# Optimization experiments

Measured on AMD Instinct MI355X. Metric: run time of the kernel, lower is better.

The kernel has to match this reference:

```python
import jax, jax.numpy as jnp
import numpy as np

V, E, H, L, B, T = 32000, 256, 512, 2, 32, 64
SOS_TOKEN = 1


def setup_inputs() -> dict:
    key = jax.random.key(0)
    ks = jax.random.split(key, 16)
    s = 0.02
    inp = {
        'encoder_outputs': jax.random.normal(ks[0], (B, T, H), dtype=jnp.float32),
        'encoder_hidden': jax.random.normal(ks[1], (L, B, H), dtype=jnp.float32),
        'target_tensor': jax.random.randint(ks[2], (B, T), 0, V, dtype=jnp.int64),
        'embedding': jax.random.normal(ks[3], (V, E), dtype=jnp.float32) * s,
        'W_ih0': jax.random.normal(ks[4], (3 * H, E), dtype=jnp.float32) * s,
        'W_hh0': jax.random.normal(ks[5], (3 * H, H), dtype=jnp.float32) * s,
        'b_ih0': jax.random.normal(ks[6], (3 * H,), dtype=jnp.float32) * s,
        'b_hh0': jax.random.normal(ks[7], (3 * H,), dtype=jnp.float32) * s,
        'W_ih1': jax.random.normal(ks[8], (3 * H, H), dtype=jnp.float32) * s,
        'W_hh1': jax.random.normal(ks[9], (3 * H, H), dtype=jnp.float32) * s,
        'b_ih1': jax.random.normal(ks[10], (3 * H,), dtype=jnp.float32) * s,
        'b_hh1': jax.random.normal(ks[11], (3 * H,), dtype=jnp.float32) * s,
        'W_out': jax.random.normal(ks[12], (V, H), dtype=jnp.float32) * s,
        'b_out': jax.random.normal(ks[13], (V,), dtype=jnp.float32) * s,
    }
    return inp


def gru_cell(x, h, W_ih, W_hh, b_ih, b_hh):
    # PyTorch GRU cell: gates ordered [r, z, n]
    gi = x @ W_ih.T + b_ih            # [B, 3H]
    gh = h @ W_hh.T + b_hh            # [B, 3H]
    i_r, i_z, i_n = jnp.split(gi, 3, axis=-1)
    h_r, h_z, h_n = jnp.split(gh, 3, axis=-1)
    r = jax.nn.sigmoid(i_r + h_r)
    z = jax.nn.sigmoid(i_z + h_z)
    n = jnp.tanh(i_n + r * h_n)
    return (1.0 - z) * n + z * h


def reference(encoder_outputs, encoder_hidden, target_tensor,
              embedding, W_ih0, W_hh0, b_ih0, b_hh0,
              W_ih1, W_hh1, b_ih1, b_hh1, W_out, b_out):
    # full teacher forcing: input token at step i is target[:, i-1], SOS at step 0
    tokens = jnp.concatenate(
        [jnp.full((B, 1), SOS_TOKEN, dtype=target_tensor.dtype),
         target_tensor[:, :-1]], axis=1)                     # [B, T]
    emb = jax.nn.relu(embedding[tokens])                     # [B, T, E]
    emb_t = jnp.swapaxes(emb, 0, 1)                          # [T, B, E]

    def step(h, x):
        h0 = gru_cell(x, h[0], W_ih0, W_hh0, b_ih0, b_hh0)
        h1 = gru_cell(h0, h[1], W_ih1, W_hh1, b_ih1, b_hh1)
        h_new = jnp.stack([h0, h1])                          # [L, B, H]
        return h_new, h1

    h_final, tops = jax.lax.scan(step, encoder_hidden, emb_t)  # tops: [T, B, H]
    logits = jnp.einsum('tbh,vh->btv', tops, W_out) + b_out    # [B, T, V]
    log_probs = jax.nn.log_softmax(logits, axis=-1)
    return log_probs, h_final
```

## Files before the change

kernel.cpp:

```cpp
#include <hip/hip_runtime.h>
#include <hip/hip_bf16.h>

namespace {

constexpr int NV = 32000;
constexpr int NE = 256;
constexpr int NH = 512;
constexpr int NB = 32;
constexpr int NT = 64;
constexpr int NG = 3 * NH;
constexpr int NM = NB * NT;
constexpr int SOS = 1;
constexpr int NTILE = 250;
constexpr int NITEM = 8 * NTILE;
constexpr int NWORK = 232;
constexpr int NV4 = NV / 4;

typedef _Float16 f16_t;
typedef _Float16 f16x8 __attribute__((ext_vector_type(8)));
typedef float f32x4 __attribute__((ext_vector_type(4)));

typedef __attribute__((address_space(1))) void gvoid_t;
typedef __attribute__((address_space(3))) void lvoid_t;

__device__ __forceinline__ int fragoff(int u, int b) {
  return ((b >> 4) * 16 + (u >> 5)) * 512 +
         ((((u >> 3) & 3) * 16) + (b & 15)) * 8 + (u & 7);
}

__device__ __forceinline__ void load_wf(const float* wrow, f16x8* wf) {
  #pragma unroll
  for (int kc = 0; kc < 16; ++kc) {
    f32x4 a = *(const f32x4*)(wrow + kc * 32);
    f32x4 c = *(const f32x4*)(wrow + kc * 32 + 4);
    f16x8 w;
    w[0] = (f16_t)a[0]; w[1] = (f16_t)a[1]; w[2] = (f16_t)a[2]; w[3] = (f16_t)a[3];
    w[4] = (f16_t)c[0]; w[5] = (f16_t)c[1]; w[6] = (f16_t)c[2]; w[7] = (f16_t)c[3];
    wf[kc] = w;
  }
}

__device__ __forceinline__ float sigm(float x) { return 1.f / (1.f + __expf(-x)); }

__device__ __forceinline__ void wait_flag(int* p, int target) {
  while (__hip_atomic_load(p, __ATOMIC_RELAXED, __HIP_MEMORY_SCOPE_AGENT) < target)
    __builtin_amdgcn_s_sleep(1);
}

__device__ __forceinline__ int peek_flag(int* p) {
  return __hip_atomic_load(p, __ATOMIC_RELAXED, __HIP_MEMORY_SCOPE_AGENT);
}

__device__ __forceinline__ void store8(void* dst, unsigned long long v) {
  __hip_atomic_store((unsigned long long*)dst, v, __ATOMIC_RELAXED,
                     __HIP_MEMORY_SCOPE_AGENT);
}


__global__ __launch_bounds__(256) void k_hinit(const float* __restrict__ eh,
                                               f16_t* __restrict__ hb0,
                                               f16_t* __restrict__ hb1) {
  int idx = blockIdx.x * 256 + threadIdx.x;
  int u = idx & 511;
  int b = (idx >> 9) & 31;
  int l = idx >> 14;
  f16_t v = (f16_t)eh[idx];
  (l ? hb1 : hb0)[fragoff(u, b)] = v;
}

__global__ __launch_bounds__(256) void k_gi0(const int* __restrict__ tgt,
                                             const float* __restrict__ emb,
                                             const float* __restrict__ Wih0,
                                             const float* __restrict__ bih0,
                                             f16_t* __restrict__ Gi0) {
  __shared__ float xs[NE * 33];
  __shared__ int toks[NB];
  const int t = blockIdx.y;
  const int tid = threadIdx.x;
  if (tid < NB) toks[tid] = (t == 0) ? SOS : tgt[tid * NT + (t - 1)];
  __syncthreads();
  #pragma unroll 4
  for (int b = 0; b < NB; ++b) {
    float v = emb[(size_t)toks[b] * NE + tid];
    xs[tid * 33 + b] = v > 0.f ? v : 0.f;
  }
  __syncthreads();
  const int b = tid & 31;
  #pragma unroll
  for (int jj = 0; jj < 8; ++jj) {
    const int j = blockIdx.x * 64 + jj * 8 + (tid >> 5);
    float acc = bih0[j];
    const f32x4* wr = (const f32x4*)(Wih0 + (size_t)j * NE);
    #pragma unroll 4
    for (int e4 = 0; e4 < NE / 4; ++e4) {
      f32x4 w = wr[e4];
      acc += w[0] * xs[(4 * e4 + 0) * 33 + b] + w[1] * xs[(4 * e4 + 1) * 33 + b]
           + w[2] * xs[(4 * e4 + 2) * 33 + b] + w[3] * xs[(4 * e4 + 3) * 33 + b];
    }
    Gi0[((size_t)t * NG + j) * NB + b] = (f16_t)acc;
  }
}


__global__ __launch_bounds__(768) void k_mega(
    const f16_t* __restrict__ Gi0,
    const float* __restrict__ Whh0, const float* __restrict__ bhh0,
    const float* __restrict__ Wih1, const float* __restrict__ bih1,
    const float* __restrict__ Whh1, const float* __restrict__ bhh1,
    const float* __restrict__ eh,
    f16_t* __restrict__ hb0, f16_t* __restrict__ hb1,
    f16_t* __restrict__ Abf, float* __restrict__ hfin,
    const float* __restrict__ Wout, const float* __restrict__ bout,
    f16_t* __restrict__ Wf, float* __restrict__ C,
    int* f0, int* f1, int* cnt, int* wflag) {
  __shared__ __align__(16) char pool[49152];
  __shared__ float red[32];
  const int tid = threadIdx.x;
  const int wave = tid >> 6, lane = tid & 63;
  const int bid = blockIdx.x;
  const int eb = tid & 31, eu0 = (tid >> 5) & 15;

  if (bid < 8) {
    float* gLDS = (float*)pool;
    f16_t* hstage = (f16_t*)(pool + 24576);
    const int ug = bid * 64;
    const int gate = wave >> 2, tile = wave & 3;
    const int row = gate * 512 + ug + tile * 16 + (lane & 15);
    f16x8 wf[16];
    load_wf(Whh0 + (size_t)row * NH + (lane >> 4) * 8, wf);

    float hprev[4], br[4], bz[4], bn[4];
    if (tid < 512) {
      #pragma unroll
      for (int i = 0; i < 4; ++i) {
        int u = ug + eu0 + i * 16;
        hprev[i] = eh[eb * NH + u];
        br[i] = bhh0[u]; bz[i] = bhh0[512 + u]; bn[i] = bhh0[1024 + u];
      }
    }

    for (int t = 0; t < NT; ++t) {
      float gr[4], gz[4], gn[4];
      if (tid < 512) {
        const f16_t* g = Gi0 + (size_t)t * NG * NB;
        #pragma unroll
        for (int i = 0; i < 4; ++i) {
          int u = ug + eu0 + i * 16;
          gr[i] = (float)g[u * NB + eb];
          gz[i] = (float)g[(512 + u) * NB + eb];
          gn[i] = (float)g[(1024 + u) * NB + eb];
        }
      }
      if (t > 0 && tid < 8) wait_flag(f0 + tid * 16, t);
      __syncthreads();
      const f16_t* hb = hb0 + (size_t)t * 16384;
      f32x4 acc0 = {0.f, 0.f, 0.f, 0.f}, acc1 = {0.f, 0.f, 0.f, 0.f};
      #pragma unroll
      for (int kc = 0; kc < 16; ++kc) {
        f16x8 b0 = *(const f16x8*)(hb + kc * 512 + lane * 8);
        f16x8 b1 = *(const f16x8*)(hb + (16 + kc) * 512 + lane * 8);
        acc0 = __builtin_amdgcn_mfma_f32_16x16x32_f16(wf[kc], b0, acc0, 0, 0, 0);
        acc1 = __builtin_amdgcn_mfma_f32_16x16x32_f16(wf[kc], b1, acc1, 0, 0, 0);
      }
      {
        const int m0 = (lane >> 4) * 4, col = lane & 15;
        #pragma unroll
        for (int r = 0; r < 4; ++r) {
          int ul = tile * 16 + m0 + r;
          gLDS[(gate * 64 + ul) * 32 + col] = acc0[r];
          gLDS[(gate * 64 + ul) * 32 + 16 + col] = acc1[r];
        }
      }
      __syncthreads();
      if (tid < 512) {
        #pragma unroll
        for (int i = 0; i < 4; ++i) {
          int ul = eu0 + i * 16;
          float rt = gLDS[(0 * 64 + ul) * 32 + eb];
          float zt = gLDS[(1 * 64 + ul) * 32 + eb];
          float nt_ = gLDS[(2 * 64 + ul) * 32 + eb];
          float r = sigm(gr[i] + rt + br[i]);
          float z = sigm(gz[i] + zt + bz[i]);
          float n = tanhf(gn[i] + r * (nt_ + bn[i]));
          float hnew = (1.f - z) * n + z * hprev[i];
          hprev[i] = hnew;
          hstage[((eb >> 4) * 2 + (ul >> 5)) * 512 +
                 ((((ul >> 3) & 3) * 16) + (eb & 15)) * 8 + (ul & 7)] = (f16_t)hnew;
          if (t == NT - 1) hfin[eb * NH + ug + ul] = hnew;
        }
      }
      __syncthreads();
      if (tid < 512) {
        const int chunk = tid >> 7, w = tid & 127;
        const unsigned long long v =
            *(const unsigned long long*)(hstage + chunk * 512 + w * 4);
        store8(hb0 + (size_t)(t + 1) * 16384 +
               ((chunk >> 1) * 16 + (ug >> 5) + (chunk & 1)) * 512 + w * 4, v);
      }
      __syncthreads();
      if (tid == 0)
        __hip_atomic_store(f0 + bid * 16, t + 1, __ATOMIC_RELEASE,
                           __HIP_MEMORY_SCOPE_AGENT);
    }
  } else if (bid < 24) {
    float* gLDS = (float*)pool;
    f16_t* hstage = (f16_t*)(pool + 24576);
    f16_t* astage = (f16_t*)(pool + 28672);
    const int g = bid - 8, ug = g * 32;
    const int mm = wave >= 6;
    const int w6 = mm ? wave - 6 : wave;
    const int gate = w6 >> 1, tile = w6 & 1;
    const int row = gate * 512 + ug + tile * 16 + (lane & 15);
    const float* W = mm ? Whh1 : Wih1;
    f16x8 wf[16];
    load_wf(W + (size_t)row * NH + (lane >> 4) * 8, wf);

    float hprev[2], bir[2], biz[2], bin_[2], bhr[2], bhz[2], bhn[2];
    if (tid < 512) {
      #pragma unroll
      for (int i = 0; i < 2; ++i) {
        int u = ug + eu0 + i * 16;
        hprev[i] = eh[16384 + eb * NH + u];
        bir[i] = bih1[u]; biz[i] = bih1[512 + u]; bin_[i] = bih1[1024 + u];
        bhr[i] = bhh1[u]; bhz[i] = bhh1[512 + u]; bhn[i] = bhh1[1024 + u];
      }
    }

    for (int t = 0; t < NT; ++t) {
      if (tid < 24) {
        int* p   = (tid < 8) ? (f0 + tid * 16) : (f1 + (tid - 8) * 16);
        int tgt  = (tid < 8) ? (t + 1) : t;
        wait_flag(p, tgt);
      }
      __syncthreads();
      const f16_t* hb = mm ? (hb1 + (size_t)t * 16384)
                           : (hb0 + (size_t)(t + 1) * 16384);
      f32x4 acc0 = {0.f, 0.f, 0.f, 0.f}, acc1 = {0.f, 0.f, 0.f, 0.f};
      #pragma unroll
      for (int kc = 0; kc < 16; ++kc) {
        f16x8 b0 = *(const f16x8*)(hb + kc * 512 + lane * 8);
        f16x8 b1 = *(const f16x8*)(hb + (16 + kc) * 512 + lane * 8);
        acc0 = __builtin_amdgcn_mfma_f32_16x16x32_f16(wf[kc], b0, acc0, 0, 0, 0);
        acc1 = __builtin_amdgcn_mfma_f32_16x16x32_f16(wf[kc], b1, acc1, 0, 0, 0);
      }
      {
        const int m0 = (lane >> 4) * 4, col = lane & 15;
        #pragma unroll
        for (int r = 0; r < 4; ++r) {
          int ul = tile * 16 + m0 + r;
          gLDS[((mm * 3 + gate) * 32 + ul) * 32 + col] = acc0[r];
          gLDS[((mm * 3 + gate) * 32 + ul) * 32 + 16 + col] = acc1[r];
        }
      }
      __syncthreads();
      if (tid < 512) {
        #pragma unroll
        for (int i = 0; i < 2; ++i) {
          int ul = eu0 + i * 16;
          float ir  = gLDS[((0 * 3 + 0) * 32 + ul) * 32 + eb] + bir[i];
          float iz  = gLDS[((0 * 3 + 1) * 32 + ul) * 32 + eb] + biz[i];
          float in_ = gLDS[((0 * 3 + 2) * 32 + ul) * 32 + eb] + bin_[i];
          float hr  = gLDS[((1 * 3 + 0) * 32 + ul) * 32 + eb] + bhr[i];
          float hz  = gLDS[((1 * 3 + 1) * 32 + ul) * 32 + eb] + bhz[i];
          float hn  = gLDS[((1 * 3 + 2) * 32 + ul) * 32 + eb] + bhn[i];
          float r = sigm(ir + hr);
          float z = sigm(iz + hz);
          float n = tanhf(in_ + r * hn);
          float hnew = (1.f - z) * n + z * hprev[i];
          hprev[i] = hnew;
          f16_t hv = (f16_t)hnew;
          hstage[(eb >> 4) * 512 +
                 ((((ul >> 3) & 3) * 16) + (eb & 15)) * 8 + (ul & 7)] = hv;
          astage[eb * 32 + ul] = hv;
          if (t == NT - 1) hfin[16384 + eb * NH + ug + ul] = hnew;
        }
      }
      __syncthreads();
      if (tid < 256) {
        const int chunk = tid >> 7, w = tid & 127;
        const unsigned long long v =
            *(const unsigned long long*)(hstage + chunk * 512 + w * 4);
        store8(hb1 + (size_t)(t + 1) * 16384 + (chunk * 16 + g) * 512 + w * 4, v);
      } else if (tid < 512) {
        const int i2 = tid - 256;
        const int b = i2 >> 3, uo = (i2 & 7) * 4;
        store8(Abf + ((size_t)(t * NB + b)) * 512 + ug + uo,
               *(const unsigned long long*)(astage + b * 32 + uo));
      }
      __syncthreads();
      if (tid == 0)
        __hip_atomic_store(f1 + g * 16, t + 1, __ATOMIC_RELEASE,
                           __HIP_MEMORY_SCOPE_AGENT);
    }
  } else {
    f16_t* AsB = (f16_t*)pool;
    f16_t* BsB = (f16_t*)(pool + 32768);
    const int wid = bid - 24;
    const int r_in = lane >> 2;
    const int c8 = (lane & 3) * 8;

    auto lsm_row = [&](int idx) {
      const int t = idx >> 5, b = idx & 31;
      f32x4* p4 = (f32x4*)(C + (size_t)(b * 64 + t) * NV);
      float mx = -3.0e38f;
      for (int i = tid; i < NV4; i += 768) {
        f32x4 v = p4[i];
        mx = fmaxf(fmaxf(fmaxf(mx, v[0]), fmaxf(v[1], v[2])), v[3]);
      }
      #pragma unroll
      for (int o = 1; o < 64; o <<= 1) mx = fmaxf(mx, __shfl_xor(mx, o, 64));
      if (lane == 0) red[wave] = mx;
      __syncthreads();
      mx = red[0];
      #pragma unroll
      for (int wv = 1; wv < 12; ++wv) mx = fmaxf(mx, red[wv]);
      float s = 0.f;
      for (int i = tid; i < NV4; i += 768) {
        f32x4 v = p4[i];
        s += __expf(v[0] - mx) + __expf(v[1] - mx) +
             __expf(v[2] - mx) + __expf(v[3] - mx);
      }
      #pragma unroll
      for (int o = 1; o < 64; o <<= 1) s += __shfl_xor(s, o, 64);
      if (lane == 0) red[16 + wave] = s;
      __syncthreads();
      s = 0.f;
      #pragma unroll
      for (int wv = 0; wv < 12; ++wv) s += red[16 + wv];
      const float lse = mx + __logf(s);
      for (int i = tid; i < NV4; i += 768) {
        f32x4 v = p4[i];
        v[0] -= lse; v[1] -= lse; v[2] -= lse; v[3] -= lse;
        p4[i] = v;
      }
      __syncthreads();
    };

    for (int tl = wid; tl < NTILE; tl += NWORK) {
      for (int i = tid; i < 128 * 512 / 8; i += 768) {
        const float* src = Wout + (size_t)tl * 128 * 512 + i * 8;
        f32x4 a = *(const f32x4*)src;
        f32x4 b = *(const f32x4*)(src + 4);
        f16x8 o;
        o[0] = (f16_t)a[0]; o[1] = (f16_t)a[1]; o[2] = (f16_t)a[2]; o[3] = (f16_t)a[3];
        o[4] = (f16_t)b[0]; o[5] = (f16_t)b[1]; o[6] = (f16_t)b[2]; o[7] = (f16_t)b[3];
        *(f16x8*)(Wf + (size_t)tl * 128 * 512 + i * 8) = o;
      }
      __syncthreads();
      if (tid == 0)
        __hip_atomic_store(wflag + tl * 16, 1, __ATOMIC_RELEASE,
                           __HIP_MEMORY_SCOPE_AGENT);
    }

    int lsmIdx = wid;

    for (int item = wid; item < NITEM; item += NWORK) {
      const int mp = item / NTILE, tl = item - mp * NTILE;
      const int m0 = mp * 256;
      const int n0 = tl * 128;
      if (tid < 16) wait_flag(f1 + tid * 16, mp * 8 + 8);
      else if (tid == 16) wait_flag(wflag + tl * 16, 1);
      __syncthreads();

      auto stage = [&](int buf, int kk) {
        if (wave < 8) {
          const f16_t* Ag = Abf + (size_t)(m0 + wave * 32 + r_in) * NH + kk + c8;
          f16_t* la = AsB + buf * 8192 + (wave * 32) * 32;
          __builtin_amdgcn_global_load_lds((gvoid_t*)Ag, (lvoid_t*)la, 16, 0, 0);
          __builtin_amdgcn_global_load_lds((gvoid_t*)(Ag + 16 * NH),
                                           (lvoid_t*)(la + 16 * 32), 16, 0, 0);
        } else {
          const f16_t* Bg = Wf + (size_t)(n0 + (wave - 8) * 32 + r_in) * NH + kk + c8;
          f16_t* lb = BsB + buf * 4096 + ((wave - 8) * 32) * 32;
          __builtin_amdgcn_global_load_lds((gvoid_t*)Bg, (lvoid_t*)lb, 16, 0, 0);
          __builtin_amdgcn_global_load_lds((gvoid_t*)(Bg + 16 * NH),
                                           (lvoid_t*)(lb + 16 * 32), 16, 0, 0);
        }
      };

      f32x4 acc[4][4];
      #pragma unroll
      for (int i = 0; i < 4; ++i)
        #pragma unroll
        for (int j = 0; j < 4; ++j)
          acc[i][j] = (f32x4){0.f, 0.f, 0.f, 0.f};

      const int wm = (wave >> 1) * 64;
      const int wn = (wave & 1) * 64;
      const int arow = lane & 15;
      const int kg = (lane >> 4) * 8;

      stage(0, 0);
      __syncthreads();
      for (int kt = 0; kt < NH / 32; ++kt) {
        const int buf = kt & 1;
        if (kt + 1 < NH / 32) stage(buf ^ 1, (kt + 1) * 32);
        if (wave < 8) {
          f16x8 af[4], bfr[4];
          #pragma unroll
          for (int i = 0; i < 4; ++i) {
            af[i]  = *(const f16x8*)&AsB[buf * 8192 + (wm + i * 16 + arow) * 32 + kg];
            bfr[i] = *(const f16x8*)&BsB[buf * 4096 + (wn + i * 16 + arow) * 32 + kg];
          }
          #pragma unroll
          for (int i = 0; i < 4; ++i)
            #pragma unroll
            for (int j = 0; j < 4; ++j)
              acc[i][j] = __builtin_amdgcn_mfma_f32_16x16x32_f16(af[i], bfr[j],
                                                                 acc[i][j], 0, 0, 0);
        }
        __syncthreads();
      }

      if (wave < 8) {
        const int crow = (lane >> 4) * 4;
        const int ccol = lane & 15;
        #pragma unroll
        for (int j = 0; j < 4; ++j) {
          const int gcol = n0 + wn + j * 16 + ccol;
          const float bb = bout[gcol];
          #pragma unroll
          for (int i = 0; i < 4; ++i) {
            #pragma unroll
            for (int r = 0; r < 4; ++r) {
              const int am = m0 + wm + i * 16 + crow + r;
              const int orow = (am & 31) * 64 + (am >> 5);
              C[(size_t)orow * NV + gcol] = acc[i][j][r] + bb;
            }
          }
        }
      }
      __syncthreads();
      if (tid == 0)
        __hip_atomic_fetch_add(cnt + mp * 16, 1, __ATOMIC_RELEASE,
                               __HIP_MEMORY_SCOPE_AGENT);

      while (lsmIdx < NM) {
        const int lvl = lsmIdx >> 8;
        if (tid == 0) red[31] = (float)(peek_flag(cnt + lvl * 16) >= NTILE);
        __syncthreads();
        const bool ready = red[31] != 0.f;
        __syncthreads();
        if (!ready) break;
        if (tid == 0) __builtin_amdgcn_fence(__ATOMIC_ACQUIRE, "agent");
        __syncthreads();
        lsm_row(lsmIdx);
        lsmIdx += NWORK;
      }
    }

    for (; lsmIdx < NM; lsmIdx += NWORK) {
      const int lvl = lsmIdx >> 8;
      if (tid == 0) {
        wait_flag(cnt + lvl * 16, NTILE);
        __builtin_amdgcn_fence(__ATOMIC_ACQUIRE, "agent");
      }
      __syncthreads();
      lsm_row(lsmIdx);
    }
  }
}

constexpr size_t WS_F0  = 0;
constexpr size_t WS_F1  = 512;
constexpr size_t WS_CNT = 1536;
constexpr size_t WS_WFL = 2048;
constexpr size_t WS_GI0 = 18432;
constexpr size_t WS_HB0 = WS_GI0 + sizeof(f16_t) * (size_t)NT * NG * NB;
constexpr size_t WS_HB1 = WS_HB0 + sizeof(f16_t) * (size_t)(NT + 1) * NH * NB;
constexpr size_t WS_ABF = WS_HB1 + sizeof(f16_t) * (size_t)(NT + 1) * NH * NB;
constexpr size_t WS_WF  = WS_ABF + sizeof(f16_t) * (size_t)NM * NH;

}

extern "C" void kernel_launch(void* const* d_in, const int* in_sizes, int n_in,
                              void* d_out, int out_size, void* d_ws, size_t ws_size,
                              hipStream_t stream) {
  const float* enc_h = (const float*)d_in[1];
  const int*   tgt   = (const int*)d_in[2];
  const float* emb   = (const float*)d_in[3];
  const float* Wih0  = (const float*)d_in[4];
  const float* Whh0  = (const float*)d_in[5];
  const float* bih0  = (const float*)d_in[6];
  const float* bhh0  = (const float*)d_in[7];
  const float* Wih1  = (const float*)d_in[8];
  const float* Whh1  = (const float*)d_in[9];
  const float* bih1  = (const float*)d_in[10];
  const float* bhh1  = (const float*)d_in[11];
  const float* Wout  = (const float*)d_in[12];
  const float* bout  = (const float*)d_in[13];

  char* ws = (char*)d_ws;
  int*    f0   = (int*)(ws + WS_F0);
  int*    f1   = (int*)(ws + WS_F1);
  int*    cnt  = (int*)(ws + WS_CNT);
  int*    wfl  = (int*)(ws + WS_WFL);
  f16_t*  Gi0  = (f16_t*)(ws + WS_GI0);
  f16_t*  hb0  = (f16_t*)(ws + WS_HB0);
  f16_t*  hb1  = (f16_t*)(ws + WS_HB1);
  f16_t*  Abf  = (f16_t*)(ws + WS_ABF);
  f16_t*  Wf   = (f16_t*)(ws + WS_WF);

  float* out  = (float*)d_out;
  float* hfin = out + (size_t)NM * NV;

  hipMemsetAsync(ws, 0, 18432, stream);
  k_hinit<<<(2 * NB * NH) / 256, 256, 0, stream>>>(enc_h, hb0, hb1);
  k_gi0<<<dim3(NG / 64, NT), 256, 0, stream>>>(tgt, emb, Wih0, bih0, Gi0);
  k_mega<<<256, 768, 0, stream>>>(Gi0, Whh0, bhh0, Wih1, bih1, Whh1, bhh1,
                                  enc_h, hb0, hb1, Abf, hfin, Wout, bout,
                                  Wf, out, f0, f1, cnt, wfl);
}
```

Baseline: 784.4 us.

## Fuse per-tile softmax statistics into output GEMM epilogue and fold h-init into mega kernel

```diff
diff --git a/kernel.cpp b/kernel.cpp
--- a/kernel.cpp
+++ b/kernel.cpp
@@ -23,6 +23,8 @@
 typedef __attribute__((address_space(1))) void gvoid_t;
 typedef __attribute__((address_space(3))) void lvoid_t;
 
+union P8 { f16_t h[4]; unsigned long long u; };
+
 __device__ __forceinline__ int fragoff(int u, int b) {
   return ((b >> 4) * 16 + (u >> 5)) * 512 +
          ((((u >> 3) & 3) * 16) + (b & 15)) * 8 + (u & 7);
@@ -56,17 +58,6 @@
                      __HIP_MEMORY_SCOPE_AGENT);
 }
 
-
-__global__ __launch_bounds__(256) void k_hinit(const float* __restrict__ eh,
-                                               f16_t* __restrict__ hb0,
-                                               f16_t* __restrict__ hb1) {
-  int idx = blockIdx.x * 256 + threadIdx.x;
-  int u = idx & 511;
-  int b = (idx >> 9) & 31;
-  int l = idx >> 14;
-  f16_t v = (f16_t)eh[idx];
-  (l ? hb1 : hb0)[fragoff(u, b)] = v;
-}
 
 __global__ __launch_bounds__(256) void k_gi0(const int* __restrict__ tgt,
                                              const float* __restrict__ emb,
@@ -112,9 +103,11 @@
     f16_t* __restrict__ Abf, float* __restrict__ hfin,
     const float* __restrict__ Wout, const float* __restrict__ bout,
     f16_t* __restrict__ Wf, float* __restrict__ C,
-    int* f0, int* f1, int* cnt, int* wflag) {
+    float* __restrict__ smax, float* __restrict__ ssum,
+    int* f0, int* f1, int* cnt, int* wflag, int* initc) {
   __shared__ __align__(16) char pool[49152];
   __shared__ float red[32];
+  __shared__ float mW[256], sW[256];
   const int tid = threadIdx.x;
   const int wave = tid >> 6, lane = tid & 63;
   const int bid = blockIdx.x;
@@ -128,6 +121,20 @@
     const int row = gate * 512 + ug + tile * 16 + (lane & 15);
     f16x8 wf[16];
     load_wf(Whh0 + (size_t)row * NH + (lane >> 4) * 8, wf);
+
+    for (int k = tid; k < 512; k += 768) {
+      const int u0 = ug + (k & 15) * 4, b = k >> 4;
+      P8 p;
+      #pragma unroll
+      for (int i = 0; i < 4; ++i) p.h[i] = (f16_t)eh[b * NH + u0 + i];
+      store8(hb0 + fragoff(u0, b), p.u);
+    }
+    __syncthreads();
+    if (tid == 0) {
+      __hip_atomic_fetch_add(initc, 1, __ATOMIC_RELEASE, __HIP_MEMORY_SCOPE_AGENT);
+      wait_flag(initc, 24);
+    }
+    __syncthreads();
 
     float hprev[4], br[4], bz[4], bn[4];
     if (tid < 512) {
@@ -214,6 +221,20 @@
     const float* W = mm ? Whh1 : Wih1;
     f16x8 wf[16];
     load_wf(W + (size_t)row * NH + (lane >> 4) * 8, wf);
+
+    for (int k = tid; k < 256; k += 768) {
+      const int u0 = ug + (k & 7) * 4, b = k >> 3;
+      P8 p;
+      #pragma unroll
+      for (int i = 0; i < 4; ++i) p.h[i] = (f16_t)eh[16384 + b * NH + u0 + i];
+      store8(hb1 + fragoff(u0, b), p.u);
+    }
+    __syncthreads();
+    if (tid == 0) {
+      __hip_atomic_fetch_add(initc, 1, __ATOMIC_RELEASE, __HIP_MEMORY_SCOPE_AGENT);
+      wait_flag(initc, 24);
+    }
+    __syncthreads();
 
     float hprev[2], bir[2], biz[2], bin_[2], bhr[2], bhz[2], bhn[2];
     if (tid < 512) {
@@ -301,33 +322,29 @@
 
     auto lsm_row = [&](int idx) {
       const int t = idx >> 5, b = idx & 31;
+      float mt = -3.0e38f, st = 0.f;
+      if (tid < NTILE) {
+        mt = smax[(size_t)idx * NTILE + tid];
+        st = ssum[(size_t)idx * NTILE + tid];
+      }
+      float m = mt;
+      #pragma unroll
+      for (int o = 1; o < 64; o <<= 1) m = fmaxf(m, __shfl_xor(m, o, 64));
+      if (lane == 0) red[wave] = m;
+      __syncthreads();
+      m = red[0];
+      #pragma unroll
+      for (int wv = 1; wv < 12; ++wv) m = fmaxf(m, red[wv]);
+      float sc = st * __expf(mt - m);
+      #pragma unroll
+      for (int o = 1; o < 64; o <<= 1) sc += __shfl_xor(sc, o, 64);
+      if (lane == 0) red[16 + wave] = sc;
+      __syncthreads();
+      float S = 0.f;
+      #pragma unroll
+      for (int wv = 0; wv < 12; ++wv) S += red[16 + wv];
+      const float lse = m + __logf(S);
       f32x4* p4 = (f32x4*)(C + (size_t)(b * 64 + t) * NV);
-      float mx = -3.0e38f;
-      for (int i = tid; i < NV4; i += 768) {
-        f32x4 v = p4[i];
-        mx = fmaxf(fmaxf(fmaxf(mx, v[0]), fmaxf(v[1], v[2])), v[3]);
-      }
-      #pragma unroll
-      for (int o = 1; o < 64; o <<= 1) mx = fmaxf(mx, __shfl_xor(mx, o, 64));
-      if (lane == 0) red[wave] = mx;
-      __syncthreads();
-      mx = red[0];
-      #pragma unroll
-      for (int wv = 1; wv < 12; ++wv) mx = fmaxf(mx, red[wv]);
-      float s = 0.f;
-      for (int i = tid; i < NV4; i += 768) {
-        f32x4 v = p4[i];
-        s += __expf(v[0] - mx) + __expf(v[1] - mx) +
-             __expf(v[2] - mx) + __expf(v[3] - mx);
-      }
-      #pragma unroll
-      for (int o = 1; o < 64; o <<= 1) s += __shfl_xor(s, o, 64);
-      if (lane == 0) red[16 + wave] = s;
-      __syncthreads();
-      s = 0.f;
-      #pragma unroll
-      for (int wv = 0; wv < 12; ++wv) s += red[16 + wv];
-      const float lse = mx + __logf(s);
       for (int i = tid; i < NV4; i += 768) {
         f32x4 v = p4[i];
         v[0] -= lse; v[1] -= lse; v[2] -= lse; v[3] -= lse;
@@ -412,23 +429,67 @@
         __syncthreads();
       }
 
+      float myM[4][4], myS[4][4];
       if (wave < 8) {
         const int crow = (lane >> 4) * 4;
         const int ccol = lane & 15;
+        float bb[4];
+        #pragma unroll
+        for (int j = 0; j < 4; ++j) bb[j] = bout[n0 + wn + j * 16 + ccol];
         #pragma unroll
         for (int j = 0; j < 4; ++j) {
           const int gcol = n0 + wn + j * 16 + ccol;
-          const float bb = bout[gcol];
           #pragma unroll
           for (int i = 0; i < 4; ++i) {
             #pragma unroll
             for (int r = 0; r < 4; ++r) {
               const int am = m0 + wm + i * 16 + crow + r;
               const int orow = (am & 31) * 64 + (am >> 5);
-              C[(size_t)orow * NV + gcol] = acc[i][j][r] + bb;
+              C[(size_t)orow * NV + gcol] = acc[i][j][r] + bb[j];
             }
           }
         }
+        #pragma unroll
+        for (int i = 0; i < 4; ++i)
+          #pragma unroll
+          for (int r = 0; r < 4; ++r) {
+            float v0 = acc[i][0][r] + bb[0], v1 = acc[i][1][r] + bb[1];
+            float v2 = acc[i][2][r] + bb[2], v3 = acc[i][3][r] + bb[3];
+            float mm2 = fmaxf(fmaxf(v0, v1), fmaxf(v2, v3));
+            #pragma unroll
+            for (int o = 1; o < 16; o <<= 1) mm2 = fmaxf(mm2, __shfl_xor(mm2, o, 64));
+            float ss = __expf(v0 - mm2) + __expf(v1 - mm2) +
+                       __expf(v2 - mm2) + __expf(v3 - mm2);
+            #pragma unroll
+            for (int o = 1; o < 16; o <<= 1) ss += __shfl_xor(ss, o, 64);
+            myM[i][r] = mm2; myS[i][r] = ss;
+          }
+      }
+      __syncthreads();
+      if (wave < 8 && (wave & 1) && (lane & 15) == 0) {
+        #pragma unroll
+        for (int i = 0; i < 4; ++i)
+          #pragma unroll
+          for (int r = 0; r < 4; ++r) {
+            int R = wm + i * 16 + (lane >> 4) * 4 + r;
+            mW[R] = myM[i][r]; sW[R] = myS[i][r];
+          }
+      }
+      __syncthreads();
+      if (wave < 8 && !(wave & 1) && (lane & 15) == 0) {
+        #pragma unroll
+        for (int i = 0; i < 4; ++i)
+          #pragma unroll
+          for (int r = 0; r < 4; ++r) {
+            int R = wm + i * 16 + (lane >> 4) * 4 + r;
+            float mo = mW[R], so = sW[R];
+            float me = myM[i][r], se = myS[i][r];
+            float M = fmaxf(me, mo);
+            float S = se * __expf(me - M) + so * __expf(mo - M);
+            int am = m0 + R;
+            smax[(size_t)am * NTILE + tl] = M;
+            ssum[(size_t)am * NTILE + tl] = S;
+          }
       }
       __syncthreads();
       if (tid == 0)
@@ -465,11 +526,14 @@
 constexpr size_t WS_F1  = 512;
 constexpr size_t WS_CNT = 1536;
 constexpr size_t WS_WFL = 2048;
+constexpr size_t WS_INI = 18048;
 constexpr size_t WS_GI0 = 18432;
 constexpr size_t WS_HB0 = WS_GI0 + sizeof(f16_t) * (size_t)NT * NG * NB;
 constexpr size_t WS_HB1 = WS_HB0 + sizeof(f16_t) * (size_t)(NT + 1) * NH * NB;
 constexpr size_t WS_ABF = WS_HB1 + sizeof(f16_t) * (size_t)(NT + 1) * NH * NB;
 constexpr size_t WS_WF  = WS_ABF + sizeof(f16_t) * (size_t)NM * NH;
+constexpr size_t WS_SM  = WS_WF + sizeof(f16_t) * (size_t)NV * NH;
+constexpr size_t WS_SS  = WS_SM + sizeof(float) * (size_t)NM * NTILE;
 
 }
 
@@ -495,19 +559,21 @@
   int*    f1   = (int*)(ws + WS_F1);
   int*    cnt  = (int*)(ws + WS_CNT);
   int*    wfl  = (int*)(ws + WS_WFL);
+  int*    ini  = (int*)(ws + WS_INI);
   f16_t*  Gi0  = (f16_t*)(ws + WS_GI0);
   f16_t*  hb0  = (f16_t*)(ws + WS_HB0);
   f16_t*  hb1  = (f16_t*)(ws + WS_HB1);
   f16_t*  Abf  = (f16_t*)(ws + WS_ABF);
   f16_t*  Wf   = (f16_t*)(ws + WS_WF);
+  float*  sm   = (float*)(ws + WS_SM);
+  float*  ss   = (float*)(ws + WS_SS);
 
   float* out  = (float*)d_out;
   float* hfin = out + (size_t)NM * NV;
 
   hipMemsetAsync(ws, 0, 18432, stream);
-  k_hinit<<<(2 * NB * NH) / 256, 256, 0, stream>>>(enc_h, hb0, hb1);
   k_gi0<<<dim3(NG / 64, NT), 256, 0, stream>>>(tgt, emb, Wih0, bih0, Gi0);
   k_mega<<<256, 768, 0, stream>>>(Gi0, Whh0, bhh0, Wih1, bih1, Whh1, bhh1,
                                   enc_h, hb0, hb1, Abf, hfin, Wout, bout,
-                                  Wf, out, f0, f1, cnt, wfl);
-}
+                                  Wf, out, sm, ss, f0, f1, cnt, wfl, ini);
+}
```

Result: no change. 779.0 us (-0.7%).
